# Optimization experiments

Measured on AMD Instinct MI355X. Metric: run time of the kernel, lower is better.

The kernel has to match this reference:

```python
import jax, jax.numpy as jnp
import numpy as np

B, C, D, J = 8, 2048, 128, 128

def setup_inputs() -> dict:
    key = jax.random.key(0)
    ks = jax.random.split(key, 24)
    s = 0.02
    inp = {
        "operation_features": jax.random.normal(ks[0], (B, C, D), jnp.float32),
        "relations": jax.random.randint(ks[1], (B, C - 2, 2), 0, C, jnp.int64),
        "begins_idx": jax.random.randint(ks[2], (B, J), 0, C, jnp.int64),
        "ends_idx": jax.random.randint(ks[3], (B, J), 0, C, jnp.int64),
        "same_type_mask": (jax.random.uniform(ks[4], (B, C, C)) > 0.5).astype(jnp.float32),
        # BeginEndEncoder
        "W_begin": jax.random.normal(ks[5], (D, D), jnp.float32) * s,
        "b_begin": jnp.zeros((D,), jnp.float32),
        "W_end": jax.random.normal(ks[6], (D, D), jnp.float32) * s,
        "b_end": jnp.zeros((D,), jnp.float32),
        # OperationTimeRelationEncoder.mix: Linear(3D -> D)
        "W_mix3": jax.random.normal(ks[7], (3 * D, D), jnp.float32) * s,
        "b_mix3": jnp.zeros((D,), jnp.float32),
        # SelfAttention (hidden_dim = D)
        "W_qkv": jax.random.normal(ks[8], (D, 3 * D), jnp.float32) * s,
        "b_qkv": jnp.zeros((3 * D,), jnp.float32),
        "w_score": jax.random.normal(ks[9], (2 * D,), jnp.float32) * s,
        "b_score": jnp.zeros((), jnp.float32),
        "W_out": jax.random.normal(ks[10], (D, D), jnp.float32) * s,
        "b_out": jnp.zeros((D,), jnp.float32),
        # block mix: Linear(2D -> D)
        "W_mix2": jax.random.normal(ks[11], (2 * D, D), jnp.float32) * s,
        "b_mix2": jnp.zeros((D,), jnp.float32),
    }
    return inp

def _gather_ops(ops, idx):
    # ops: [B,C,D], idx: [B,M] -> [B,M,D]  (torch.gather along dim 1 with expanded index)
    Bb, _, Dd = ops.shape
    M = idx.shape[1]
    return jnp.take_along_axis(ops, jnp.broadcast_to(idx[:, :, None], (Bb, M, Dd)), axis=1)

def reference(operation_features, relations, begins_idx, ends_idx, same_type_mask,
              W_begin, b_begin, W_end, b_end, W_mix3, b_mix3,
              W_qkv, b_qkv, w_score, b_score, W_out, b_out, W_mix2, b_mix2):
    ops = operation_features
    Dd = ops.shape[-1]
    # --- OperationTimeRelationEncoder ---
    pred = _gather_ops(ops, relations[..., 0])      # [B,C-2,D]
    succ = _gather_ops(ops, relations[..., 1])      # [B,C-2,D]
    concated = jnp.concatenate([ops[:, :-2, :], pred, succ], axis=-1)  # [B,C-2,3D]
    mixed = concated @ W_mix3 + b_mix3              # [B,C-2,D]
    begin_f = _gather_ops(ops, begins_idx) @ W_begin + b_begin  # [B,J,D]
    end_f = _gather_ops(ops, ends_idx) @ W_end + b_end
    begin = jnp.mean(begin_f, axis=1)               # [B,D]
    end = jnp.mean(end_f, axis=1)
    seq = jnp.concatenate([mixed, begin[:, None, :], end[:, None, :]], axis=1)  # [B,C,D]
    # --- SelfAttention (GAT-style additive score, decomposed to avoid CxCx2h blowup) ---
    qkv = ops @ W_qkv + b_qkv                       # [B,C,3D]
    q, k, v = jnp.split(qkv, 3, axis=-1)
    sq = q @ w_score[:Dd]                           # [B,C]  q_i . w_q
    sk = k @ w_score[Dd:]                           # [B,C]  k_j . w_k
    scores = jax.nn.leaky_relu(sq[:, :, None] + sk[:, None, :] + b_score)  # [B,C,C]
    attn = jax.nn.softmax(scores * same_type_mask, axis=-1)                # multiplicative mask, as in torch
    weighted = jnp.einsum('bij,bjd->bid', attn, v)  # [B,C,D]
    same_type = weighted @ W_out + b_out            # [B,C,D]
    # --- final mix ---
    return jnp.concatenate([seq, same_type], axis=-1) @ W_mix2 + b_mix2  # [B,C,D]
```

## Files before the change

### kernel.cpp

```cpp
#include <hip/hip_runtime.h>
#include <cstddef>

typedef __bf16 bf16;
typedef __bf16 bf16x4 __attribute__((ext_vector_type(4)));
typedef __bf16 bf16x8 __attribute__((ext_vector_type(8)));
typedef float  f32x4  __attribute__((ext_vector_type(4)));

#define MFMA16(a, b, c) __builtin_amdgcn_mfma_f32_16x16x32_bf16((a), (b), (c), 0, 0, 0)

#define BB 8
#define CC 2048
#define DD 128
#define JJN 128

#define WS_PK    ((size_t)0)
#define WS_OPS16 ((size_t)8388608)
#define WS_SQF   ((size_t)12582912)
#define WS_SKF   ((size_t)12648448)
#define WS_G1T   ((size_t)12713984)
#define WS_G2T   ((size_t)12746752)
#define WS_G3T   ((size_t)12779520)
#define WS_WCT   ((size_t)12812288)
#define WS_GBT   ((size_t)12845056)
#define WS_GET   ((size_t)12877824)
#define WS_UQK   ((size_t)12910592)
#define WS_BBM   ((size_t)12911104)
#define WS_BBB   ((size_t)12911616)
#define WS_BBE   ((size_t)12912128)
#define WS_SC    ((size_t)12912640)
#define WS_WCN   ((size_t)12913152)
#define WS_GBN   ((size_t)12945920)
#define WS_GEN   ((size_t)12978688)
#define WS_MB    ((size_t)13011456)
#define WS_MEANV ((size_t)17205760)

__global__ __launch_bounds__(256) void k_prepcast(
    const float* __restrict__ ops, bf16* __restrict__ ops16,
    const int* __restrict__ begins, const int* __restrict__ ends,
    const float* __restrict__ Wmix3, const float* __restrict__ Wmix2,
    const float* __restrict__ Wout,  const float* __restrict__ Wbegin,
    const float* __restrict__ Wend,  const float* __restrict__ Wqkv,
    const float* __restrict__ bqkv,  const float* __restrict__ wscore,
    const float* __restrict__ bscore,const float* __restrict__ bmix3,
    const float* __restrict__ bout,  const float* __restrict__ bmix2,
    const float* __restrict__ bbegin,const float* __restrict__ bend,
    bf16* __restrict__ G1T, bf16* __restrict__ G2T, bf16* __restrict__ G3T,
    bf16* __restrict__ WCT, bf16* __restrict__ GBT, bf16* __restrict__ GET,
    bf16* __restrict__ WCN, bf16* __restrict__ GBN, bf16* __restrict__ GEN,
    bf16* __restrict__ uqk, float* __restrict__ BBM, float* __restrict__ BBB,
    float* __restrict__ BBE, float* __restrict__ sc, float* __restrict__ MEANV)
{
    __shared__ bf16  LshT[128 * 132];
    __shared__ float Rsh[128 * 8];
    int wg = blockIdx.x;
    int t  = threadIdx.x;

    if (wg == 0) {
        for (int half = 0; half < 2; ++half) {
            #pragma unroll
            for (int pass = 0; pass < 16; ++pass) {
                int idx = pass * 256 + t;
                int d   = idx >> 5;
                int e0  = (idx & 31) * 4;
                f32x4 v = *(const f32x4*)(Wqkv + d*384 + half*128 + e0);
                #pragma unroll
                for (int jj = 0; jj < 4; ++jj)
                    LshT[(e0 + jj)*132 + d] = (bf16)v[jj];
            }
            if (t < 32) {
                f32x4 wv = *(const f32x4*)(wscore + half*128 + t*4);
                #pragma unroll
                for (int jj = 0; jj < 4; ++jj) Rsh[t*4 + jj] = wv[jj];
            }
            __syncthreads();
            if (t < 128) {
                float s = 0.f;
                for (int e = 0; e < 128; ++e)
                    s += (float)LshT[e*132 + t] * Rsh[e];
                uqk[half*128 + t] = (bf16)s;
            }
            __syncthreads();
        }
        float bm = 0.f, bb_ = 0.f, be_ = 0.f, bon = 0.f;
        for (int half = 0; half < 2; ++half) {
            #pragma unroll
            for (int pass = 0; pass < 16; ++pass) {
                int idx = pass * 256 + t;
                int f   = idx >> 5;
                int e0  = (idx & 31) * 4;
                f32x4 v = *(const f32x4*)(Wmix2 + (size_t)(half*128 + f)*128 + e0);
                #pragma unroll
                for (int jj = 0; jj < 4; ++jj)
                    LshT[f*132 + e0 + jj] = (bf16)v[jj];
            }
            if (t < 32) {
                if (half == 0) {
                    f32x4 v0 = *(const f32x4*)(bmix3  + t*4);
                    f32x4 v1 = *(const f32x4*)(bbegin + t*4);
                    f32x4 v2 = *(const f32x4*)(bend   + t*4);
                    #pragma unroll
                    for (int jj = 0; jj < 4; ++jj) {
                        Rsh[t*4 + jj]       = v0[jj];
                        Rsh[128 + t*4 + jj] = v1[jj];
                        Rsh[256 + t*4 + jj] = v2[jj];
                    }
                } else {
                    f32x4 v3 = *(const f32x4*)(bout + t*4);
                    #pragma unroll
                    for (int jj = 0; jj < 4; ++jj) Rsh[t*4 + jj] = v3[jj];
                }
            }
            __syncthreads();
            if (t < 128) {
                if (half == 0) {
                    for (int f = 0; f < 128; ++f) {
                        float wv = (float)LshT[f*132 + t];
                        bm  += Rsh[f]       * wv;
                        bb_ += Rsh[128 + f] * wv;
                        be_ += Rsh[256 + f] * wv;
                    }
                } else {
                    for (int f = 0; f < 128; ++f)
                        bon += Rsh[f] * (float)LshT[f*132 + t];
                }
            }
            __syncthreads();
        }
        if (t < 128) {
            float bm2 = bmix2[t];
            BBM[t] = bm  + bon + bm2;
            BBB[t] = bb_ + bon + bm2;
            BBE[t] = be_ + bon + bm2;
        }
        if (t >= 128) {
            int e2 = t - 128;
            Rsh[512 + e2] = bqkv[e2]       * wscore[e2];
            Rsh[640 + e2] = bqkv[128 + e2] * wscore[128 + e2];
        }
        __syncthreads();
        if (t == 0) {
            float cq = 0.f, ck = 0.f;
            for (int e2 = 0; e2 < 128; ++e2) {
                cq += Rsh[512 + e2];
                ck += Rsh[640 + e2];
            }
            sc[0] = cq + bscore[0];
            sc[1] = ck;
        }
        return;
    }
    if (wg <= 16) {
        int task = wg - 1;
        int b2 = task >> 1, which = task & 1;
        const int* idxp = which ? (ends + b2 * JJN) : (begins + b2 * JJN);
        int* ish = (int*)Rsh;
        if (t < JJN) ish[t] = idxp[t];
        __syncthreads();
        int d = t & 127, half = t >> 7;
        const float* opsb = ops + (size_t)b2 * CC * DD;
        float s = 0.f;
        #pragma unroll 8
        for (int j = 0; j < 64; ++j) {
            int r = ish[half * 64 + j];
            s += opsb[(size_t)r * DD + d];
        }
        float* fsh = Rsh + 256;
        fsh[half * 128 + d] = s;
        __syncthreads();
        if (t < 128)
            MEANV[task * 128 + t] = (fsh[t] + fsh[128 + t]) * (1.0f / (float)JJN);
        return;
    }
    if (wg <= 112) {
        int id  = wg - 17;
        int mat = id >> 4, sub = id & 15;
        const float* L; const float* R; bf16* O; bf16* O2;
        switch (mat) {
            case 0: L = Wmix3;           R = Wmix2;           O = G1T; O2 = nullptr; break;
            case 1: L = Wmix3 + 128*128; R = Wmix2;           O = G2T; O2 = nullptr; break;
            case 2: L = Wmix3 + 256*128; R = Wmix2;           O = G3T; O2 = nullptr; break;
            case 3: L = Wout;            R = Wmix2 + 128*128; O = WCT; O2 = WCN; break;
            case 4: L = Wbegin;          R = Wmix2;           O = GBT; O2 = GBN; break;
            default:L = Wend;            R = Wmix2;           O = GET; O2 = GEN; break;
        }
        int e0 = sub * 8;
        #pragma unroll
        for (int pass = 0; pass < 16; ++pass) {
            int idx = pass * 256 + t;
            int d   = idx >> 5;
            int f0  = (idx & 31) * 4;
            f32x4 v = *(const f32x4*)(L + d * 128 + f0);
            #pragma unroll
            for (int jj = 0; jj < 4; ++jj)
                LshT[(f0 + jj) * 132 + d] = (bf16)v[jj];
        }
        #pragma unroll
        for (int pass = 0; pass < 4; ++pass) {
            int idx = pass * 256 + t;
            int f   = idx >> 3;
            int ee  = idx & 7;
            Rsh[f * 8 + ee] = R[f * 128 + e0 + ee];
        }
        __syncthreads();
        int ee = t >> 5;
        int e  = e0 + ee;
        int d0 = (t & 31) * 4;
        float s[4] = {0.f, 0.f, 0.f, 0.f};
        for (int f = 0; f < 128; ++f) {
            bf16x4 lv = *(const bf16x4*)&LshT[f * 132 + d0];
            float rv = Rsh[f * 8 + ee];
            #pragma unroll
            for (int dd = 0; dd < 4; ++dd)
                s[dd] += (float)lv[dd] * rv;
        }
        #pragma unroll
        for (int dd = 0; dd < 4; ++dd) {
            O[e * 128 + d0 + dd] = (bf16)s[dd];
            if (O2) O2[(d0 + dd) * 128 + e] = (bf16)s[dd];
        }
        return;
    }
    size_t i = (size_t)(wg - 113) * 256 + t;
    f32x4 a = *(const f32x4*)(ops + i * 8);
    f32x4 b = *(const f32x4*)(ops + i * 8 + 4);
    bf16x8 o;
    #pragma unroll
    for (int e = 0; e < 4; ++e) { o[e] = (bf16)a[e]; o[4 + e] = (bf16)b[e]; }
    *(bf16x8*)(ops16 + i * 8) = o;
}

__global__ __launch_bounds__(256) void k_v(
    const bf16* __restrict__ ops16, const float* __restrict__ Wqkv,
    const float* __restrict__ bqkv, const bf16* __restrict__ uqk,
    const float* __restrict__ sc,   const float* __restrict__ mask,
    bf16* __restrict__ PK, float* __restrict__ sqf, float* __restrict__ skf,
    unsigned char* __restrict__ MBITS)
{
    __shared__ bf16 A[144 * 136];
    int t = threadIdx.x;
    if (blockIdx.x >= 256) {
        int p = blockIdx.x - 256;
        size_t base = (size_t)p * 16384;
        const float* mp = mask + base;
        unsigned char* ob = MBITS + (base >> 3);
        #pragma unroll
        for (int k = 0; k < 8; ++k) {
            size_t fo = (size_t)k * 2048 + (size_t)t * 8;
            f32x4 a = __builtin_nontemporal_load((const f32x4*)(mp + fo));
            f32x4 c = __builtin_nontemporal_load((const f32x4*)(mp + fo + 4));
            unsigned byte = 0;
            #pragma unroll
            for (int e = 0; e < 4; ++e) {
                byte |= (a[e] != 0.f ? 1u : 0u) << e;
                byte |= (c[e] != 0.f ? 1u : 0u) << (4 + e);
            }
            ob[k * 256 + t] = (unsigned char)byte;
        }
        return;
    }
    int b  = blockIdx.x & 7;
    int jt = (blockIdx.x >> 3) * 64;
    #pragma unroll
    for (int pass = 0; pass < 16; ++pass) {
        int idx = pass * 256 + t;
        int d   = idx >> 5;
        int n0  = (idx & 31) * 4;
        f32x4 v = *(const f32x4*)(Wqkv + d*384 + 256 + n0);
        #pragma unroll
        for (int jj = 0; jj < 4; ++jj)
            A[(n0 + jj)*136 + d] = (bf16)v[jj];
    }
    {
        int row = t >> 7, col = t & 127;
        A[(128 + row)*136 + col] = uqk[row*128 + col];
    }
    for (int idx = t; idx < 14*136; idx += 256)
        A[130*136 + idx] = (bf16)0.f;
    __syncthreads();

    int lane = t & 63, w = t >> 6;
    int m = lane & 15, q = lane >> 4;
    f32x4 acc[9];
    #pragma unroll
    for (int rb = 0; rb < 9; ++rb) acc[rb] = {0.f, 0.f, 0.f, 0.f};

    const bf16* opsb = ops16 + (size_t)b * CC * DD;
    int j = jt + w*16 + m;
    #pragma unroll
    for (int kc = 0; kc < 4; ++kc) {
        bf16x8 bfr = *(const bf16x8*)(opsb + (size_t)j*DD + kc*32 + q*8);
        #pragma unroll
        for (int rb = 0; rb < 9; ++rb) {
            bf16x8 afr = *(const bf16x8*)&A[(rb*16 + m)*136 + kc*32 + q*8];
            acc[rb] = MFMA16(afr, bfr, acc[rb]);
        }
    }
    float cqb = sc[0], ckv = sc[1];
    if (q == 0) {
        sqf[b*CC + j] = acc[8][0] + cqb;
        skf[b*CC + j] = acc[8][1] + ckv;
    }
    __syncthreads();
    bf16* pack = A;
    {
        int jcl = w >> 1;
        int qv  = (w & 1) * 2 + (m >> 3);
        int ev  = m & 7;
        #pragma unroll
        for (int rb = 0; rb < 8; ++rb) {
            #pragma unroll
            for (int r = 0; r < 4; ++r) {
                float v = acc[rb][r] + bqkv[256 + rb*16 + q*4 + r];
                pack[jcl*4096 + rb*512 + qv*128 + (q*4+r)*8 + ev] = (bf16)v;
            }
        }
    }
    __syncthreads();
    bf16* pkb = PK + (size_t)b * DD * CC + (size_t)jt * 128;
    #pragma unroll
    for (int pass = 0; pass < 4; ++pass) {
        int lidx = pass * 256 + t;
        *(uint4*)(pkb + (size_t)lidx * 8) = *(const uint4*)&pack[lidx * 8];
    }
}

__device__ __forceinline__ void load_vb(const bf16* __restrict__ pkb, int jc,
                                        int q, int m, bf16x8 vb[8])
{
    #pragma unroll
    for (int nb = 0; nb < 8; ++nb)
        vb[nb] = *(const bf16x8*)(pkb + ((size_t)(((jc*8 + nb)*4 + q)*16 + m)) * 8);
}

__global__ __launch_bounds__(512, 2) void k_attepi(
    const unsigned char* __restrict__ MBITS, const bf16* __restrict__ PK,
    const float* __restrict__ sqf, const float* __restrict__ skf,
    const bf16* __restrict__ ops16, const int* __restrict__ relations,
    const bf16* __restrict__ G1T, const bf16* __restrict__ G2T,
    const bf16* __restrict__ G3T, const bf16* __restrict__ WCT,
    const bf16* __restrict__ GBN, const bf16* __restrict__ GEN,
    const bf16* __restrict__ WCN,
    const float* __restrict__ BBM, const float* __restrict__ BBB,
    const float* __restrict__ BBE, const float* __restrict__ MEANV,
    float* __restrict__ out)
{
    __shared__ __align__(16) char smem[52224];
    int t    = threadIdx.x;
    int lane = t & 63, w = t >> 6;
    int b    = blockIdx.x & 7;
    int i0   = (blockIdx.x >> 3) << 5;
    int m = lane & 15, q = lane >> 4;
    int tl = w & 1;
    int jg = w >> 1;

    unsigned char* Lb  = (unsigned char*)smem;
    float*         skw = (float*)(smem + 8704);

    {
        int row = t >> 4, seg = t & 15;
        *(uint4*)(Lb + row * 272 + seg * 16) = *(const uint4*)(MBITS
            + ((size_t)(b * CC + i0 + row)) * 256 + seg * 16);
    }
    *(f32x4*)(skw + t * 4) = *(const f32x4*)(skf + b * CC + t * 4);

    float sq = sqf[b * CC + i0 + tl * 16 + m];
    const bf16* pkb = PK + (size_t)b * DD * CC;
    const float* skg = skw + jg * 512;

    f32x4 acc[8];
    #pragma unroll
    for (int nb = 0; nb < 8; ++nb) acc[nb] = {0.f, 0.f, 0.f, 0.f};
    float lsum = 0.f;
    __syncthreads();

    #pragma unroll
    for (int c = 0; c < 16; ++c) {
        int jc = jg * 16 + c;
        bf16x8 vb[8];
        load_vb(pkb, jc, q, m, vb);
        unsigned mb = Lb[(tl * 16 + m) * 272 + jc * 4 + q];
        int jo = c * 32 + q * 8;
        f32x4 s0 = *(const f32x4*)(skg + jo);
        f32x4 s1 = *(const f32x4*)(skg + jo + 4);
        float sks[8] = {s0[0], s0[1], s0[2], s0[3], s1[0], s1[1], s1[2], s1[3]};
        bf16x8 a;
        #pragma unroll
        for (int e = 0; e < 8; ++e) {
            float tv = sq + sks[e];
            float lr = fmaxf(tv, 0.01f * tv);
            float p  = __expf(lr * (float)((mb >> e) & 1u));
            lsum += p;
            a[e] = (bf16)p;
        }
        #pragma unroll
        for (int nb = 0; nb < 8; ++nb)
            acc[nb] = MFMA16(a, vb[nb], acc[nb]);
    }

    lsum += __shfl_xor(lsum, 16, 64);
    lsum += __shfl_xor(lsum, 32, 64);

    __syncthreads();

    float* Osh  = (float*)(smem + 8704);
    float* Lsh  = (float*)(smem + 42496);
    bf16*  Obuf = (bf16*)(smem + 43520);
    {
        int plane = jg & 1;
        int orow  = plane * 32 + tl * 16;
        if (jg < 2) {
            if (q == 0) Lsh[plane * 32 + tl * 16 + m] = lsum;
            #pragma unroll
            for (int nb = 0; nb < 8; ++nb)
                #pragma unroll
                for (int r = 0; r < 4; ++r)
                    Osh[(orow + q * 4 + r) * 132 + nb * 16 + m] = acc[nb][r];
        }
        __syncthreads();
        if (jg >= 2) {
            if (q == 0) Lsh[plane * 32 + tl * 16 + m] += lsum;
            #pragma unroll
            for (int nb = 0; nb < 8; ++nb)
                #pragma unroll
                for (int r = 0; r < 4; ++r)
                    Osh[(orow + q * 4 + r) * 132 + nb * 16 + m] += acc[nb][r];
        }
        __syncthreads();
        int r   = t >> 4;
        int c0e = (t & 15) * 8;
        float l = Lsh[r] + Lsh[32 + r];
        float inv = 1.0f / l;
        bf16x8 o;
        #pragma unroll
        for (int e = 0; e < 8; ++e) {
            float s = Osh[r * 132 + c0e + e] + Osh[(32 + r) * 132 + c0e + e];
            o[e] = (bf16)(s * inv);
        }
        *(bf16x8*)&Obuf[r * 136 + c0e] = o;
        __syncthreads();
    }

    bf16* Abuf = (bf16*)smem;
    bf16* Bbuf = (bf16*)(smem + 8704);

    f32x4 eacc[2];
    eacc[0] = {0.f, 0.f, 0.f, 0.f};
    eacc[1] = {0.f, 0.f, 0.f, 0.f};

    const bf16* Bsrc[4] = {G1T, G2T, G3T, WCT};
    int arow = t >> 4, ao = (t & 15) * 8;
    int brow = t >> 2, bo2 = (t & 3) * 32;
    int c = i0 + arow;

    for (int term = 0; term < 4; ++term) {
        if (term < 3) {
            const bf16* src;
            if (term == 0) src = ops16 + ((size_t)(b * CC + c)) * DD;
            else {
                int ridx = relations[((size_t)b * (CC - 2) + min(c, CC - 3)) * 2 + (term - 1)];
                src = ops16 + ((size_t)(b * CC) + ridx) * DD;
            }
            *(uint4*)&Abuf[arow * 136 + ao] = *(const uint4*)(src + ao);
        }
        #pragma unroll
        for (int ii = 0; ii < 4; ++ii)
            *(uint4*)&Bbuf[brow * 136 + bo2 + ii*8] =
                *(const uint4*)(Bsrc[term] + brow * 128 + bo2 + ii*8);
        __syncthreads();

        const bf16* Asrc = (term == 3) ? Obuf : Abuf;
        #pragma unroll
        for (int kc = 0; kc < 4; ++kc) {
            bf16x8 bfr = *(const bf16x8*)&Bbuf[(w*16 + m)*136 + kc*32 + q*8];
            #pragma unroll
            for (int rb = 0; rb < 2; ++rb) {
                bf16x8 afr = *(const bf16x8*)&Asrc[(rb*16 + m)*136 + kc*32 + q*8];
                eacc[rb] = MFMA16(afr, bfr, eacc[rb]);
            }
        }
        __syncthreads();
    }
    {
        int col = w*16 + m;
        float bias = BBM[col];
        #pragma unroll
        for (int rb = 0; rb < 2; ++rb) {
            #pragma unroll
            for (int r = 0; r < 4; ++r) {
                int cg = i0 + rb*16 + q*4 + r;
                if (cg < CC - 2)
                    out[((size_t)(b * CC) + cg) * DD + col] = eacc[rb][r] + bias;
            }
        }
    }

    if (i0 == CC - 32) {
        __syncthreads();
        float* mv2 = (float*)smem;
        if (t < 256)
            mv2[(t >> 7) * 128 + (t & 127)] =
                MEANV[((size_t)b * 2 + (t >> 7)) * 128 + (t & 127)];
        __syncthreads();
        if (t < 256) {
            int grp = t >> 7, tlx = t & 127;
            int which = grp;
            const bf16* G    = which ? GEN : GBN;
            const float* Bv  = which ? BBE : BBB;
            const bf16* orow = Obuf + (30 + which) * 136;
            float a = Bv[tlx];
            const float* mv = mv2 + grp * 128;
            for (int d = 0; d < 128; ++d) {
                a += mv[d] * (float)G[d * 128 + tlx];
                a += (float)orow[d] * (float)WCN[d * 128 + tlx];
            }
            out[((size_t)b * CC + (CC - 2 + which)) * DD + tlx] = a;
        }
    }
}

extern "C" void kernel_launch(void* const* d_in, const int* in_sizes, int n_in,
                              void* d_out, int out_size, void* d_ws, size_t ws_size,
                              hipStream_t stream)
{
    const float* ops      = (const float*)d_in[0];
    const int*  relations = (const int*)d_in[1];
    const int*  begins    = (const int*)d_in[2];
    const int*  ends      = (const int*)d_in[3];
    const float* mask     = (const float*)d_in[4];
    const float* Wbegin   = (const float*)d_in[5];
    const float* bbegin   = (const float*)d_in[6];
    const float* Wend     = (const float*)d_in[7];
    const float* bend     = (const float*)d_in[8];
    const float* Wmix3    = (const float*)d_in[9];
    const float* bmix3    = (const float*)d_in[10];
    const float* Wqkv     = (const float*)d_in[11];
    const float* bqkv     = (const float*)d_in[12];
    const float* wscore   = (const float*)d_in[13];
    const float* bscore   = (const float*)d_in[14];
    const float* Wout     = (const float*)d_in[15];
    const float* bout     = (const float*)d_in[16];
    const float* Wmix2    = (const float*)d_in[17];
    const float* bmix2    = (const float*)d_in[18];
    float* outp = (float*)d_out;

    char* ws = (char*)d_ws;
    bf16*  PK    = (bf16*)(ws + WS_PK);
    bf16*  OPS16 = (bf16*)(ws + WS_OPS16);
    float* sqf   = (float*)(ws + WS_SQF);
    float* skf   = (float*)(ws + WS_SKF);
    bf16*  G1T   = (bf16*)(ws + WS_G1T);
    bf16*  G2T   = (bf16*)(ws + WS_G2T);
    bf16*  G3T   = (bf16*)(ws + WS_G3T);
    bf16*  WCT   = (bf16*)(ws + WS_WCT);
    bf16*  GBT   = (bf16*)(ws + WS_GBT);
    bf16*  GET   = (bf16*)(ws + WS_GET);
    bf16*  WCN   = (bf16*)(ws + WS_WCN);
    bf16*  GBN   = (bf16*)(ws + WS_GBN);
    bf16*  GEN   = (bf16*)(ws + WS_GEN);
    bf16*  UQK   = (bf16*)(ws + WS_UQK);
    float* BBM   = (float*)(ws + WS_BBM);
    float* BBB   = (float*)(ws + WS_BBB);
    float* BBE   = (float*)(ws + WS_BBE);
    float* SC    = (float*)(ws + WS_SC);
    unsigned char* MBITS = (unsigned char*)(ws + WS_MB);
    float* MEANV = (float*)(ws + WS_MEANV);

    k_prepcast<<<dim3(1137), dim3(256), 0, stream>>>(
        ops, OPS16, begins, ends,
        Wmix3, Wmix2, Wout, Wbegin, Wend, Wqkv, bqkv, wscore, bscore,
        bmix3, bout, bmix2, bbegin, bend,
        G1T, G2T, G3T, WCT, GBT, GET, WCN, GBN, GEN,
        UQK, BBM, BBB, BBE, SC, MEANV);

    k_v<<<dim3(2304), dim3(256), 0, stream>>>(
        OPS16, Wqkv, bqkv, UQK, SC, mask, PK, sqf, skf, MBITS);

    k_attepi<<<dim3(512), dim3(512), 0, stream>>>(
        MBITS, PK, sqf, skf, OPS16, relations,
        G1T, G2T, G3T, WCT, GBN, GEN, WCN, BBM, BBB, BBE, MEANV, outp);
}
```

Baseline: 279.5 us.

## Split attention over key halves into separate kernel, epilogue merges partials

The fused attention+epilogue kernel is split in two. k_att runs 1024 blocks, each covering half of the key range, and writes unnormalised fp32 partial outputs and row sums to workspace. A new k_epi kernel with 256 threads combines the two halves, normalises, and runs the mixing GEMM with a 2x2 MFMA tile per wave. The goal is more parallelism on 256 CUs and a lighter, separate epilogue. The cost is an extra kernel launch and an fp32 partial round trip through global memory (about 32 MB).

```diff
diff --git a/kernel.cpp b/kernel.cpp
--- a/kernel.cpp
+++ b/kernel.cpp
@@ -33,6 +33,8 @@
 #define WS_GEN   ((size_t)12978688)
 #define WS_MB    ((size_t)13011456)
 #define WS_MEANV ((size_t)17205760)
+#define WS_PARTO ((size_t)33554432)
+#define WS_PARTL ((size_t)50331648)
 
 __global__ __launch_bounds__(256) void k_prepcast(
     const float* __restrict__ ops, bf16* __restrict__ ops16,
@@ -332,9 +334,115 @@
         vb[nb] = *(const bf16x8*)(pkb + ((size_t)(((jc*8 + nb)*4 + q)*16 + m)) * 8);
 }
 
-__global__ __launch_bounds__(512, 2) void k_attepi(
+__global__ __launch_bounds__(512, 2) void k_att(
     const unsigned char* __restrict__ MBITS, const bf16* __restrict__ PK,
     const float* __restrict__ sqf, const float* __restrict__ skf,
+    float* __restrict__ PARTO, float* __restrict__ PARTL)
+{
+    __shared__ __align__(16) char smem[34048];
+    int t    = threadIdx.x;
+    int lane = t & 63, w = t >> 6;
+    int b    = blockIdx.x & 7;
+    int it   = (blockIdx.x >> 3) & 63;
+    int jh   = blockIdx.x >> 9;
+    int i0   = it << 5;
+    int m = lane & 15, q = lane >> 4;
+    int tl = w & 1;
+    int jg = w >> 1;
+
+    unsigned char* Lb  = (unsigned char*)smem;
+    float*         skw = (float*)(smem + 4352);
+
+    {
+        int row = t >> 4, seg = t & 15;
+        *(uint2*)(Lb + row * 136 + seg * 8) = *(const uint2*)(MBITS
+            + ((size_t)(b * CC + i0 + row)) * 256 + jh * 128 + seg * 8);
+    }
+    if (t < 256)
+        *(f32x4*)(skw + t * 4) = *(const f32x4*)(skf + b * CC + jh * 1024 + t * 4);
+
+    float sq = sqf[b * CC + i0 + tl * 16 + m];
+    const bf16* pkb = PK + (size_t)b * DD * CC;
+    const float* skg = skw + jg * 256;
+
+    f32x4 acc[8];
+    #pragma unroll
+    for (int nb = 0; nb < 8; ++nb) acc[nb] = {0.f, 0.f, 0.f, 0.f};
+    float lsum = 0.f;
+    __syncthreads();
+
+    #pragma unroll
+    for (int c = 0; c < 8; ++c) {
+        int jcl = jg * 8 + c;
+        int jc  = jh * 32 + jcl;
+        bf16x8 vb[8];
+        load_vb(pkb, jc, q, m, vb);
+        unsigned mb = Lb[(tl * 16 + m) * 136 + jcl * 4 + q];
+        int jo = c * 32 + q * 8;
+        f32x4 s0 = *(const f32x4*)(skg + jo);
+        f32x4 s1 = *(const f32x4*)(skg + jo + 4);
+        float sks[8] = {s0[0], s0[1], s0[2], s0[3], s1[0], s1[1], s1[2], s1[3]};
+        bf16x8 a;
+        #pragma unroll
+        for (int e = 0; e < 8; ++e) {
+            float tv = sq + sks[e];
+            float lr = fmaxf(tv, 0.01f * tv);
+            float p  = __expf(lr * (float)((mb >> e) & 1u));
+            lsum += p;
+            a[e] = (bf16)p;
+        }
+        #pragma unroll
+        for (int nb = 0; nb < 8; ++nb)
+            acc[nb] = MFMA16(a, vb[nb], acc[nb]);
+    }
+
+    lsum += __shfl_xor(lsum, 16, 64);
+    lsum += __shfl_xor(lsum, 32, 64);
+
+    __syncthreads();
+
+    float* Osh = (float*)smem;
+    float* Lsh = (float*)(smem + 33792);
+    {
+        int plane = jg & 1;
+        int orow  = plane * 32 + tl * 16;
+        if (jg < 2) {
+            if (q == 0) Lsh[plane * 32 + tl * 16 + m] = lsum;
+            #pragma unroll
+            for (int nb = 0; nb < 8; ++nb)
+                #pragma unroll
+                for (int r = 0; r < 4; ++r)
+                    Osh[(orow + q * 4 + r) * 132 + nb * 16 + m] = acc[nb][r];
+        }
+        __syncthreads();
+        if (jg >= 2) {
+            if (q == 0) Lsh[plane * 32 + tl * 16 + m] += lsum;
+            #pragma unroll
+            for (int nb = 0; nb < 8; ++nb)
+                #pragma unroll
+                for (int r = 0; r < 4; ++r)
+                    Osh[(orow + q * 4 + r) * 132 + nb * 16 + m] += acc[nb][r];
+        }
+        __syncthreads();
+        int r   = t >> 4;
+        int c0e = (t & 15) * 8;
+        size_t idx = (size_t)((b * 64 + it) * 2 + jh);
+        float* po = PARTO + idx * 4096;
+        f32x4 o0, o1;
+        #pragma unroll
+        for (int e = 0; e < 4; ++e) {
+            o0[e] = Osh[r * 132 + c0e + e]     + Osh[(32 + r) * 132 + c0e + e];
+            o1[e] = Osh[r * 132 + c0e + 4 + e] + Osh[(32 + r) * 132 + c0e + 4 + e];
+        }
+        *(f32x4*)(po + r * 128 + c0e)     = o0;
+        *(f32x4*)(po + r * 128 + c0e + 4) = o1;
+        if ((t & 15) == 0)
+            PARTL[idx * 32 + r] = Lsh[r] + Lsh[32 + r];
+    }
+}
+
+__global__ __launch_bounds__(256) void k_epi(
+    const float* __restrict__ PARTO, const float* __restrict__ PARTL,
     const bf16* __restrict__ ops16, const int* __restrict__ relations,
     const bf16* __restrict__ G1T, const bf16* __restrict__ G2T,
     const bf16* __restrict__ G3T, const bf16* __restrict__ WCT,
@@ -345,111 +453,48 @@
     float* __restrict__ out)
 {
     __shared__ __align__(16) char smem[52224];
-    int t    = threadIdx.x;
+    int t  = threadIdx.x;
     int lane = t & 63, w = t >> 6;
-    int b    = blockIdx.x & 7;
-    int i0   = (blockIdx.x >> 3) << 5;
+    int b  = blockIdx.x & 7;
+    int it = blockIdx.x >> 3;
+    int i0 = it << 5;
     int m = lane & 15, q = lane >> 4;
-    int tl = w & 1;
-    int jg = w >> 1;
-
-    unsigned char* Lb  = (unsigned char*)smem;
-    float*         skw = (float*)(smem + 8704);
-
+
+    float* Lsh0 = (float*)smem;
+    bf16*  Obuf = (bf16*)(smem + 43520);
+    int base2 = (b * 64 + it) * 2;
+    if (t < 64) Lsh0[t] = PARTL[base2 * 32 + t];
+    __syncthreads();
     {
-        int row = t >> 4, seg = t & 15;
-        *(uint4*)(Lb + row * 272 + seg * 16) = *(const uint4*)(MBITS
-            + ((size_t)(b * CC + i0 + row)) * 256 + seg * 16);
-    }
-    *(f32x4*)(skw + t * 4) = *(const f32x4*)(skf + b * CC + t * 4);
-
-    float sq = sqf[b * CC + i0 + tl * 16 + m];
-    const bf16* pkb = PK + (size_t)b * DD * CC;
-    const float* skg = skw + jg * 512;
-
-    f32x4 acc[8];
-    #pragma unroll
-    for (int nb = 0; nb < 8; ++nb) acc[nb] = {0.f, 0.f, 0.f, 0.f};
-    float lsum = 0.f;
+        const float* P0 = PARTO + (size_t)base2 * 4096;
+        #pragma unroll
+        for (int pass = 0; pass < 4; ++pass) {
+            int idx = pass * 1024 + t * 4;
+            int r = idx >> 7, cc2 = idx & 127;
+            f32x4 v0 = *(const f32x4*)(P0 + r * 128 + cc2);
+            f32x4 v1 = *(const f32x4*)(P0 + 4096 + r * 128 + cc2);
+            float inv = 1.0f / (Lsh0[r] + Lsh0[32 + r]);
+            bf16x4 o;
+            #pragma unroll
+            for (int e = 0; e < 4; ++e) o[e] = (bf16)((v0[e] + v1[e]) * inv);
+            *(bf16x4*)&Obuf[r * 136 + cc2] = o;
+        }
+    }
     __syncthreads();
-
-    #pragma unroll
-    for (int c = 0; c < 16; ++c) {
-        int jc = jg * 16 + c;
-        bf16x8 vb[8];
-        load_vb(pkb, jc, q, m, vb);
-        unsigned mb = Lb[(tl * 16 + m) * 272 + jc * 4 + q];
-        int jo = c * 32 + q * 8;
-        f32x4 s0 = *(const f32x4*)(skg + jo);
-        f32x4 s1 = *(const f32x4*)(skg + jo + 4);
-        float sks[8] = {s0[0], s0[1], s0[2], s0[3], s1[0], s1[1], s1[2], s1[3]};
-        bf16x8 a;
-        #pragma unroll
-        for (int e = 0; e < 8; ++e) {
-            float tv = sq + sks[e];
-            float lr = fmaxf(tv, 0.01f * tv);
-            float p  = __expf(lr * (float)((mb >> e) & 1u));
-            lsum += p;
-            a[e] = (bf16)p;
-        }
-        #pragma unroll
-        for (int nb = 0; nb < 8; ++nb)
-            acc[nb] = MFMA16(a, vb[nb], acc[nb]);
-    }
-
-    lsum += __shfl_xor(lsum, 16, 64);
-    lsum += __shfl_xor(lsum, 32, 64);
-
-    __syncthreads();
-
-    float* Osh  = (float*)(smem + 8704);
-    float* Lsh  = (float*)(smem + 42496);
-    bf16*  Obuf = (bf16*)(smem + 43520);
-    {
-        int plane = jg & 1;
-        int orow  = plane * 32 + tl * 16;
-        if (jg < 2) {
-            if (q == 0) Lsh[plane * 32 + tl * 16 + m] = lsum;
-            #pragma unroll
-            for (int nb = 0; nb < 8; ++nb)
-                #pragma unroll
-                for (int r = 0; r < 4; ++r)
-                    Osh[(orow + q * 4 + r) * 132 + nb * 16 + m] = acc[nb][r];
-        }
-        __syncthreads();
-        if (jg >= 2) {
-            if (q == 0) Lsh[plane * 32 + tl * 16 + m] += lsum;
-            #pragma unroll
-            for (int nb = 0; nb < 8; ++nb)
-                #pragma unroll
-                for (int r = 0; r < 4; ++r)
-                    Osh[(orow + q * 4 + r) * 132 + nb * 16 + m] += acc[nb][r];
-        }
-        __syncthreads();
-        int r   = t >> 4;
-        int c0e = (t & 15) * 8;
-        float l = Lsh[r] + Lsh[32 + r];
-        float inv = 1.0f / l;
-        bf16x8 o;
-        #pragma unroll
-        for (int e = 0; e < 8; ++e) {
-            float s = Osh[r * 132 + c0e + e] + Osh[(32 + r) * 132 + c0e + e];
-            o[e] = (bf16)(s * inv);
-        }
-        *(bf16x8*)&Obuf[r * 136 + c0e] = o;
-        __syncthreads();
-    }
 
     bf16* Abuf = (bf16*)smem;
     bf16* Bbuf = (bf16*)(smem + 8704);
 
-    f32x4 eacc[2];
-    eacc[0] = {0.f, 0.f, 0.f, 0.f};
-    eacc[1] = {0.f, 0.f, 0.f, 0.f};
+    f32x4 eacc[2][2];
+    #pragma unroll
+    for (int rb = 0; rb < 2; ++rb)
+        #pragma unroll
+        for (int cb = 0; cb < 2; ++cb)
+            eacc[rb][cb] = {0.f, 0.f, 0.f, 0.f};
 
     const bf16* Bsrc[4] = {G1T, G2T, G3T, WCT};
-    int arow = t >> 4, ao = (t & 15) * 8;
-    int brow = t >> 2, bo2 = (t & 3) * 32;
+    int arow = t >> 3, ao = (t & 7) * 16;
+    int brow = t >> 1, bo2 = (t & 1) * 64;
     int c = i0 + arow;
 
     for (int term = 0; term < 4; ++term) {
@@ -460,36 +505,42 @@
                 int ridx = relations[((size_t)b * (CC - 2) + min(c, CC - 3)) * 2 + (term - 1)];
                 src = ops16 + ((size_t)(b * CC) + ridx) * DD;
             }
-            *(uint4*)&Abuf[arow * 136 + ao] = *(const uint4*)(src + ao);
-        }
-        #pragma unroll
-        for (int ii = 0; ii < 4; ++ii)
-            *(uint4*)&Bbuf[brow * 136 + bo2 + ii*8] =
-                *(const uint4*)(Bsrc[term] + brow * 128 + bo2 + ii*8);
+            *(uint4*)&Abuf[arow * 136 + ao]     = *(const uint4*)(src + ao);
+            *(uint4*)&Abuf[arow * 136 + ao + 8] = *(const uint4*)(src + ao + 8);
+        }
+        const uint4* bs = (const uint4*)(Bsrc[term] + brow * 128 + bo2);
+        uint4* bd = (uint4*)&Bbuf[brow * 136 + bo2];
+        #pragma unroll
+        for (int ii = 0; ii < 8; ++ii) bd[ii] = bs[ii];
         __syncthreads();
 
         const bf16* Asrc = (term == 3) ? Obuf : Abuf;
         #pragma unroll
         for (int kc = 0; kc < 4; ++kc) {
-            bf16x8 bfr = *(const bf16x8*)&Bbuf[(w*16 + m)*136 + kc*32 + q*8];
+            bf16x8 bfr[2];
+            #pragma unroll
+            for (int cb = 0; cb < 2; ++cb)
+                bfr[cb] = *(const bf16x8*)&Bbuf[(w * 32 + cb * 16 + m) * 136 + kc * 32 + q * 8];
             #pragma unroll
             for (int rb = 0; rb < 2; ++rb) {
-                bf16x8 afr = *(const bf16x8*)&Asrc[(rb*16 + m)*136 + kc*32 + q*8];
-                eacc[rb] = MFMA16(afr, bfr, eacc[rb]);
-            }
-        }
-        __syncthreads();
-    }
-    {
-        int col = w*16 + m;
+                bf16x8 afr = *(const bf16x8*)&Asrc[(rb * 16 + m) * 136 + kc * 32 + q * 8];
+                eacc[rb][0] = MFMA16(afr, bfr[0], eacc[rb][0]);
+                eacc[rb][1] = MFMA16(afr, bfr[1], eacc[rb][1]);
+            }
+        }
+        __syncthreads();
+    }
+    #pragma unroll
+    for (int cb = 0; cb < 2; ++cb) {
+        int col = w * 32 + cb * 16 + m;
         float bias = BBM[col];
         #pragma unroll
         for (int rb = 0; rb < 2; ++rb) {
             #pragma unroll
             for (int r = 0; r < 4; ++r) {
-                int cg = i0 + rb*16 + q*4 + r;
+                int cg = i0 + rb * 16 + q * 4 + r;
                 if (cg < CC - 2)
-                    out[((size_t)(b * CC) + cg) * DD + col] = eacc[rb][r] + bias;
+                    out[((size_t)(b * CC) + cg) * DD + col] = eacc[rb][cb][r] + bias;
             }
         }
     }
@@ -497,24 +548,20 @@
     if (i0 == CC - 32) {
         __syncthreads();
         float* mv2 = (float*)smem;
-        if (t < 256)
-            mv2[(t >> 7) * 128 + (t & 127)] =
-                MEANV[((size_t)b * 2 + (t >> 7)) * 128 + (t & 127)];
-        __syncthreads();
-        if (t < 256) {
-            int grp = t >> 7, tlx = t & 127;
-            int which = grp;
-            const bf16* G    = which ? GEN : GBN;
-            const float* Bv  = which ? BBE : BBB;
-            const bf16* orow = Obuf + (30 + which) * 136;
-            float a = Bv[tlx];
-            const float* mv = mv2 + grp * 128;
-            for (int d = 0; d < 128; ++d) {
-                a += mv[d] * (float)G[d * 128 + tlx];
-                a += (float)orow[d] * (float)WCN[d * 128 + tlx];
-            }
-            out[((size_t)b * CC + (CC - 2 + which)) * DD + tlx] = a;
-        }
+        int grp = t >> 7, tlx = t & 127;
+        mv2[grp * 128 + tlx] = MEANV[((size_t)b * 2 + grp) * 128 + tlx];
+        __syncthreads();
+        int which = grp;
+        const bf16* G    = which ? GEN : GBN;
+        const float* Bv  = which ? BBE : BBB;
+        const bf16* orow = Obuf + (30 + which) * 136;
+        float a = Bv[tlx];
+        const float* mv = mv2 + grp * 128;
+        for (int d = 0; d < 128; ++d) {
+            a += mv[d] * (float)G[d * 128 + tlx];
+            a += (float)orow[d] * (float)WCN[d * 128 + tlx];
+        }
+        out[((size_t)b * CC + (CC - 2 + which)) * DD + tlx] = a;
     }
 }
 
@@ -564,6 +611,8 @@
     float* SC    = (float*)(ws + WS_SC);
     unsigned char* MBITS = (unsigned char*)(ws + WS_MB);
     float* MEANV = (float*)(ws + WS_MEANV);
+    float* PARTO = (float*)(ws + WS_PARTO);
+    float* PARTL = (float*)(ws + WS_PARTL);
 
     k_prepcast<<<dim3(1137), dim3(256), 0, stream>>>(
         ops, OPS16, begins, ends,
@@ -575,7 +624,10 @@
     k_v<<<dim3(2304), dim3(256), 0, stream>>>(
         OPS16, Wqkv, bqkv, UQK, SC, mask, PK, sqf, skf, MBITS);
 
-    k_attepi<<<dim3(512), dim3(512), 0, stream>>>(
-        MBITS, PK, sqf, skf, OPS16, relations,
+    k_att<<<dim3(1024), dim3(512), 0, stream>>>(
+        MBITS, PK, sqf, skf, PARTO, PARTL);
+
+    k_epi<<<dim3(512), dim3(256), 0, stream>>>(
+        PARTO, PARTL, OPS16, relations,
         G1T, G2T, G3T, WCT, GBN, GEN, WCN, BBM, BBB, BBE, MEANV, outp);
 }
```

Result: slower. 287.7 us (+3.0%).
